# Performance work log

Measured on AMD Instinct MI355X. Metric: run time of the kernel, lower is better.

Reference implementation:

```python
import jax, jax.numpy as jnp
import numpy as np
from jax import lax

P = 2        # conv padding = (Fconv-1)//2 with Fconv=5
T = 10       # relaxation steps (args.T)
PRED_T = 6   # pred_inp_size=[6]: store activations after step 6

def rho(x):
    # hard-sigmoid activation used by the EP model
    return jnp.clip(x, 0.0, 1.0)

def conv2d(x, w, b=None):
    # x: [B,Cin,H,W], w: [Cout,Cin,k,k]
    y = lax.conv_general_dilated(x, w, (1, 1), [(P, P), (P, P)],
                                 dimension_numbers=('NCHW', 'OIHW', 'NCHW'))
    return y if b is None else y + b[None, :, None, None]

def maxpool2x2(x):
    # non-overlapping 2x2 max pool with per-window argmax indices
    B, C, H, W = x.shape
    xr = x.reshape(B, C, H // 2, 2, W // 2, 2).transpose(0, 1, 2, 4, 3, 5)
    xr = xr.reshape(B, C, H // 2, W // 2, 4)
    return jnp.max(xr, axis=-1), jnp.argmax(xr, axis=-1)

def unpool2x2(x, idx):
    # scatter pooled values back to the argmax position in each 2x2 window
    B, C, h, w = x.shape
    y = x[..., None] * jax.nn.one_hot(idx, 4, dtype=x.dtype)  # [B,C,h,w,4]
    return y.reshape(B, C, h, w, 2, 2).transpose(0, 1, 2, 4, 3, 5).reshape(B, C, 2 * h, 2 * w)

def _run(data, s0, s1, s2, conv0_w, conv0_b, conv1_w, conv1_b, fc_w, fc_b):
    B = data.shape[0]
    # conv_transpose2d(x, W, padding=P) == conv2d(x, flip(W).swap(O,I), padding=k-1-P); k=5,P=2 -> pad 2
    tw = jnp.flip(conv0_w, (2, 3)).transpose(1, 0, 2, 3)  # [Cin=64, Cout=128, 5, 5]
    st0 = st1 = st2 = None
    for t in range(T):
        # all dsdt computed from the pre-update states (as in torch stepper)
        d0 = -s0 + rho(s1.reshape(B, -1) @ fc_w.T + fc_b)
        p1, idx1 = maxpool2x2(conv2d(s2, conv0_w, conv0_b))            # [B,128,8,8]
        d1 = -s1 + rho(p1 + (s0 @ fc_w).reshape(s1.shape))              # top-down via fc weight
        p2, _ = maxpool2x2(conv2d(data, conv1_w, conv1_b))             # [B,64,16,16]
        up = conv2d(unpool2x2(s1, idx1), tw)                            # unpool->conv_transpose, [B,64,16,16]
        d2 = -s2 + rho(p2 + up)
        s0, s1, s2 = s0 + d0, s1 + d1, s2 + d2
        if t == PRED_T:  # store_all_activations at pred_inp_size steps
            st0, st1, st2 = s0[..., None], s1[..., None], s2[..., None]
    return s0, s1, s2, st0, st1, st2

def setup_inputs():
    key = jax.random.key(0)
    ks = jax.random.split(key, 6)
    B = 64
    f32 = jnp.float32
    return {
        'data': jax.random.normal(ks[0], (B, 3, 32, 32), f32),
        's0': jnp.zeros((B, 10), f32),
        's1': jnp.zeros((B, 128, 8, 8), f32),
        's2': jnp.zeros((B, 64, 16, 16), f32),
        'conv0_w': jax.random.normal(ks[1], (128, 64, 5, 5), f32) * 0.025,   # ~1/sqrt(64*25)
        'conv0_b': jax.random.normal(ks[2], (128,), f32) * 0.01,
        'conv1_w': jax.random.normal(ks[3], (64, 3, 5, 5), f32) * 0.115,     # ~1/sqrt(75)
        'conv1_b': jax.random.normal(ks[4], (64,), f32) * 0.01,
        'fc_w': jax.random.normal(ks[5], (10, 8192), f32) * 0.011,           # ~1/sqrt(8192)
        'fc_b': jnp.zeros((10,), f32),
    }

def reference(data, s0, s1, s2, conv0_w, conv0_b, conv1_w, conv1_b, fc_w, fc_b):
    return _run(data, s0, s1, s2, conv0_w, conv0_b, conv1_w, conv1_b, fc_w, fc_b)
```

## Files before the change

### kernel.cpp

```cpp
#include <hip/hip_runtime.h>


typedef _Float16 half8 __attribute__((ext_vector_type(8)));
typedef _Float16 half4 __attribute__((ext_vector_type(4)));
typedef _Float16 half2v __attribute__((ext_vector_type(2)));
typedef float f32x4 __attribute__((ext_vector_type(4)));
#define MFMA_F16(A, B, C) __builtin_amdgcn_mfma_f32_16x16x32_f16((A), (B), (C), 0, 0, 0)
#define LO_SCALE 2.44140625e-4f

static __device__ __forceinline__ float rho_(float x) {
  return fminf(fmaxf(x, 0.0f), 1.0f);
}
static __device__ __forceinline__ void split2(float v, _Float16& h, _Float16& l) {
  if (fabsf(v) < 6.1035156e-5f) {
    h = (_Float16)0.f;
    l = (_Float16)(v * 4096.f);
  } else {
    h = (_Float16)v;
    l = (_Float16)((v - (float)h) * 4096.f);
  }
}

__global__ __launch_bounds__(256) void k_wprep(
    const float* __restrict__ w0, const float* __restrict__ fcb,
    const float* __restrict__ fcw,
    _Float16* __restrict__ wA0h, _Float16* __restrict__ wA0l,
    _Float16* __restrict__ wA1h, _Float16* __restrict__ wA1l,
    float* __restrict__ fcwp, float* __restrict__ s0part) {
  int i = blockIdx.x * 256 + threadIdx.x;
  if (i >= 204800) return;
  if (i < 10240) {
    int k = i - (i / 10) * 10;
    s0part[i] = (i < 640) ? -fcb[k] : 0.f;
  }
  if (i < 98304) {
    int jj = i / 12, k = i - jj * 12;
    int cgpyq = jj >> 10, idx = jj & 1023;
    int cgp = cgpyq >> 2, yq = cgpyq & 3;
    int co = idx & 31, win = (idx >> 5) & 15, cgl2 = idx >> 9;
    int co_g = cgp * 64 + cgl2 * 32 + co;
    int phl = win >> 3, pw = win & 7;
    int ph = yq * 2 + phl;
    int j = co_g * 64 + ph * 8 + pw;
    fcwp[i] = (k < 10) ? fcw[k * 8192 + j] : 0.f;
  }
  {
    int cik = i & 31, t1 = i >> 5;
    int co = t1 & 127, t2 = t1 >> 7;
    int ck = t2 & 1, tap = t2 >> 1;
    float v = w0[(co * 64 + ck * 32 + cik) * 25 + tap];
    _Float16 h, l; split2(v, h, l);
    wA0h[i] = h; wA0l[i] = l;
  }
  {
    int cpk = i & 31, t1 = i >> 5;
    int o = t1 & 63, t2 = t1 >> 6;
    int c = t2 & 3, tap = t2 >> 2;
    float v = w0[((c * 32 + cpk) * 64 + o) * 25 + tap];
    _Float16 h, l; split2(v, h, l);
    wA1h[i] = h; wA1l[i] = l;
  }
}

__global__ __launch_bounds__(256) void k_p2(
    const float* __restrict__ data, const float* __restrict__ w,
    const float* __restrict__ bias, float* __restrict__ p2t) {
  __shared__ float ld[3][36][36];
  __shared__ float lw[16][80];
  __shared__ float lb[16];
  int b = blockIdx.x, cg = blockIdx.y, tid = threadIdx.x;
  for (int i = tid; i < 3 * 36 * 36; i += 256) {
    int ci = i / 1296, rem = i % 1296, y = rem / 36, x = rem % 36;
    int gy = y - 2, gx = x - 2;
    float v = 0.f;
    if (gy >= 0 && gy < 32 && gx >= 0 && gx < 32)
      v = data[(b * 3 + ci) * 1024 + gy * 32 + gx];
    ld[ci][y][x] = v;
  }
  for (int i = tid; i < 16 * 75; i += 256) {
    int co = i / 75, k = i % 75;
    lw[co][k] = w[(cg * 16 + co) * 75 + k];
  }
  if (tid < 16) lb[tid] = bias[cg * 16 + tid];
  __syncthreads();
  int ph = tid >> 4, pw = tid & 15;
  int ry = 2 * ph, rx = 2 * pw;
  for (int co = 0; co < 16; co++) {
    float bv = lb[co];
    float a00 = bv, a01 = bv, a10 = bv, a11 = bv;
    for (int ci = 0; ci < 3; ci++) {
#pragma unroll
      for (int ky = 0; ky < 5; ky++) {
#pragma unroll
        for (int kx = 0; kx < 5; kx++) {
          float wv = lw[co][(ci * 5 + ky) * 5 + kx];
          a00 += wv * ld[ci][ry + ky][rx + kx];
          a01 += wv * ld[ci][ry + ky][rx + kx + 1];
          a10 += wv * ld[ci][ry + ky + 1][rx + kx];
          a11 += wv * ld[ci][ry + ky + 1][rx + kx + 1];
        }
      }
    }
    float m = fmaxf(fmaxf(a00, a01), fmaxf(a10, a11));
    p2t[b * 16384 + tid * 64 + cg * 16 + co] = m;
  }
}

__global__ __launch_bounds__(512, 4) void k_conv0F(
    const unsigned* __restrict__ s2pk,
    const _Float16* __restrict__ wA0h, const _Float16* __restrict__ wA0l,
    const float* __restrict__ b0,
    const float* __restrict__ s1old,
    const float* __restrict__ s0prevPart, float* __restrict__ s0curPart,
    const float* __restrict__ fcb,
    const float* __restrict__ fcwp, float* __restrict__ s1new,
    float* __restrict__ s1out,
    unsigned* __restrict__ u) {
  __shared__ __align__(16) _Float16 sm[18576];
  __shared__ float s0l[10];
  __shared__ float s0red[8][10];
  int b = blockIdx.x, cgp = blockIdx.y, yq = blockIdx.z, tid = threadIdx.x;

  if (tid < 10) {
    float s = 0.f;
#pragma unroll
    for (int sl = 0; sl < 8; sl++) s += s0prevPart[(sl * 64 + b) * 10 + tid];
    s0l[tid] = rho_(s + fcb[tid]);
  }

#pragma unroll
  for (int it = 0; it < 4; it++) {
    int idx = it * 512 + tid;
    int ci4 = (idx & 15) * 4;
    int pos = idx >> 4;
    int gy = yq * 4 - 2 + (pos >> 4);
    int lx = pos & 15;
    uint4 pk = {0u, 0u, 0u, 0u};
    if ((unsigned)gy < 16u) pk = *(const uint4*)&s2pk[b * 16384 + (gy * 16 + lx) * 64 + ci4];
    half2v h0 = __builtin_bit_cast(half2v, pk.x);
    half2v h1 = __builtin_bit_cast(half2v, pk.y);
    half2v h2 = __builtin_bit_cast(half2v, pk.z);
    half2v h3 = __builtin_bit_cast(half2v, pk.w);
    half4 hi, lo;
    hi[0] = h0[0]; hi[1] = h1[0]; hi[2] = h2[0]; hi[3] = h3[0];
    lo[0] = h0[1]; lo[1] = h1[1]; lo[2] = h2[1]; lo[3] = h3[1];
    *(half4*)(sm + pos * 72 + ci4) = hi;
    *(half4*)(sm + 9288 + pos * 72 + ci4) = lo;
  }
  if (tid < 72) {
    sm[9216 + tid] = (_Float16)0.f;
    sm[9288 + 9216 + tid] = (_Float16)0.f;
  }
  __syncthreads();

  int lane = tid & 63, w = tid >> 6;
  int kc = w & 1, cgl = (w >> 1) & 1, tg = w >> 2;
  int l16 = lane & 15, quad = lane >> 4;

  f32x4 acch[4][2], accl[4][2];
#pragma unroll
  for (int nt = 0; nt < 4; nt++)
#pragma unroll
    for (int mt = 0; mt < 2; mt++) {
      f32x4 z; z[0] = 0.f; z[1] = 0.f; z[2] = 0.f; z[3] = 0.f;
      acch[nt][mt] = z; accl[nt][mt] = z;
    }

  const int bofs = kc * 32 + quad * 8;
  const int Abase = (kc * 128 + (cgp * 2 + cgl) * 32 + l16) * 32 + quad * 8;
  const int tapLo = tg ? 13 : 0;
  const int tapEnd = tg ? 25 : 13;

  half8 ahc[2], alc[2];
#pragma unroll
  for (int mt = 0; mt < 2; mt++) {
    ahc[mt] = *(const half8*)(wA0h + Abase + tapLo * 8192 + mt * 512);
    alc[mt] = *(const half8*)(wA0l + Abase + tapLo * 8192 + mt * 512);
  }

  for (int tap = tapLo; tap < tapEnd; tap++) {
    half8 ahn[2], aln[2];
    {
      int tn = (tap + 1 < tapEnd) ? tap + 1 : tap;
#pragma unroll
      for (int mt = 0; mt < 2; mt++) {
        ahn[mt] = *(const half8*)(wA0h + Abase + tn * 8192 + mt * 512);
        aln[mt] = *(const half8*)(wA0l + Abase + tn * 8192 + mt * 512);
      }
    }
    int ky = tap / 5, kx = tap - ky * 5;
    int ix = l16 + kx - 2;
    bool oob = ((unsigned)ix > 15u);
#pragma unroll
    for (int nt = 0; nt < 4; nt++) {
      int pos = (nt + ky) * 16 + ix;
      if (oob) pos = 128;
      const _Float16* bp = sm + pos * 72 + bofs;
      half8 bh = *(const half8*)bp;
      half8 bl = *(const half8*)(bp + 9288);
#pragma unroll
      for (int mt = 0; mt < 2; mt++) {
        acch[nt][mt] = MFMA_F16(ahc[mt], bh, acch[nt][mt]);
        accl[nt][mt] = MFMA_F16(alc[mt], bh, accl[nt][mt]);
        accl[nt][mt] = MFMA_F16(ahc[mt], bl, accl[nt][mt]);
      }
    }
#pragma unroll
    for (int mt = 0; mt < 2; mt++) { ahc[mt] = ahn[mt]; alc[mt] = aln[mt]; }
  }

  __syncthreads();
  float* C = (float*)sm;
  if (kc == 1) {
    float* Cw = C + (cgl * 2 + tg) * 2144;
#pragma unroll
    for (int nt = 0; nt < 4; nt++) {
      int pos = nt * 16 + l16;
#pragma unroll
      for (int mt = 0; mt < 2; mt++)
#pragma unroll
        for (int r = 0; r < 4; r++)
          Cw[(mt * 16 + quad * 4 + r) * 67 + pos] = acch[nt][mt][r] + LO_SCALE * accl[nt][mt][r];
    }
  }
  __syncthreads();
  if (kc == 0) {
    float* Cw = C + (cgl * 2 + tg) * 2144;
#pragma unroll
    for (int nt = 0; nt < 4; nt++) {
      int pos = nt * 16 + l16;
#pragma unroll
      for (int mt = 0; mt < 2; mt++)
#pragma unroll
        for (int r = 0; r < 4; r++) {
          int a = (mt * 16 + quad * 4 + r) * 67 + pos;
          Cw[a] += acch[nt][mt][r] + LO_SCALE * accl[nt][mt][r];
        }
    }
  }
  __syncthreads();

  float pacc[10];
#pragma unroll
  for (int k = 0; k < 10; k++) pacc[k] = 0.f;

#pragma unroll
  for (int it2 = 0; it2 < 2; it2++) {
    int idx = it2 * 512 + tid;
    int co = idx & 31, win = (idx >> 5) & 15, cgl2 = idx >> 9;
    int phl = win >> 3, pw = win & 7;
    int p0 = phl * 32 + pw * 2;
    int cbase = cgl2 * 4288;
    int co_g = cgp * 64 + cgl2 * 32 + co;
    float bv = b0[co_g];
    float v[4];
#pragma unroll
    for (int q = 0; q < 4; q++) {
      int ci = co * 67 + p0 + (q >> 1) * 16 + (q & 1);
      float s = C[cbase + ci] + C[cbase + 2144 + ci];
      v[q] = s + bv;
    }
    float m0 = v[0]; int id = 0;
    if (v[1] > m0) { m0 = v[1]; id = 1; }
    if (v[2] > m0) { m0 = v[2]; id = 2; }
    if (v[3] > m0) { m0 = v[3]; id = 3; }
    int ph = yq * 2 + phl;
    int jj = ((cgp * 4 + yq) << 10) + idx;
    int j = co_g * 64 + ph * 8 + pw;
    float sv = s1old[b * 8192 + jj];
    const float4* fp = (const float4*)(fcwp + jj * 12);
    float4 f0 = fp[0], f1 = fp[1], f2 = fp[2];
    float wv[10] = {f0.x, f0.y, f0.z, f0.w, f1.x, f1.y, f1.z, f1.w, f2.x, f2.y};
    float a = m0;
#pragma unroll
    for (int k = 0; k < 10; k++) {
      a += s0l[k] * wv[k];
      pacc[k] += sv * wv[k];
    }
    float r1 = rho_(a);
    s1new[b * 8192 + jj] = r1;
    if (s1out) s1out[b * 8192 + j] = r1;
    _Float16 hh, hl; split2(sv, hh, hl);
    half2v hv; hv[0] = hh; hv[1] = hl;
    unsigned pk = __builtin_bit_cast(unsigned, hv);
    int bu = (b * 256 + ph * 32 + pw * 2) * 128 + co_g;
    u[bu]        = (id == 0) ? pk : 0u;
    u[bu + 128]  = (id == 1) ? pk : 0u;
    u[bu + 2048] = (id == 2) ? pk : 0u;
    u[bu + 2176] = (id == 3) ? pk : 0u;
  }

#pragma unroll
  for (int k = 0; k < 10; k++) {
    float vv = pacc[k];
#pragma unroll
    for (int off = 32; off > 0; off >>= 1) vv += __shfl_xor(vv, off);
    if (lane == 0) s0red[w][k] = vv;
  }
  __syncthreads();
  if (tid < 10) {
    float s = s0red[0][tid] + s0red[1][tid] + s0red[2][tid] + s0red[3][tid]
            + s0red[4][tid] + s0red[5][tid] + s0red[6][tid] + s0red[7][tid];
    s0curPart[((cgp * 4 + yq) * 64 + b) * 10 + tid] = s;
  }
}

__global__ __launch_bounds__(512, 4) void k_convTF(
    const unsigned* __restrict__ u,
    const _Float16* __restrict__ wA1h, const _Float16* __restrict__ wA1l,
    const float* __restrict__ p2t, unsigned* __restrict__ s2pk) {
  __shared__ __align__(16) _Float16 sm[35088];
  int b = blockIdx.x, oh = blockIdx.y, yq = blockIdx.z, tid = threadIdx.x;

#pragma unroll
  for (int it = 0; it < 8; it++) {
    int idx = it * 512 + tid;
    int cp4 = (idx & 31) * 4;
    int pl = idx >> 5;
    int gy = yq * 4 - 2 + (pl >> 4);
    int lx = pl & 15;
    uint4 pk = {0u, 0u, 0u, 0u};
    if ((unsigned)gy < 16u) pk = *(const uint4*)&u[b * 32768 + (gy * 16 + lx) * 128 + cp4];
    half2v h0 = __builtin_bit_cast(half2v, pk.x);
    half2v h1 = __builtin_bit_cast(half2v, pk.y);
    half2v h2 = __builtin_bit_cast(half2v, pk.z);
    half2v h3 = __builtin_bit_cast(half2v, pk.w);
    half4 hi, lo;
    hi[0] = h0[0]; hi[1] = h1[0]; hi[2] = h2[0]; hi[3] = h3[0];
    lo[0] = h0[1]; lo[1] = h1[1]; lo[2] = h2[1]; lo[3] = h3[1];
    *(half4*)(sm + pl * 136 + cp4) = hi;
    *(half4*)(sm + 17544 + pl * 136 + cp4) = lo;
  }
  if (tid < 68) {
    ((unsigned*)sm)[8704 + tid] = 0u;
    ((unsigned*)sm)[8772 + 8704 + tid] = 0u;
  }
  __syncthreads();

  int lane = tid & 63, w = tid >> 6;
  int kc = w & 1, tg = w >> 1;
  int l16 = lane & 15, quad = lane >> 4;

  f32x4 acch[4][2], accl[4][2];
#pragma unroll
  for (int nt = 0; nt < 4; nt++)
#pragma unroll
    for (int mt = 0; mt < 2; mt++) {
      f32x4 z; z[0] = 0.f; z[1] = 0.f; z[2] = 0.f; z[3] = 0.f;
      acch[nt][mt] = z; accl[nt][mt] = z;
    }

  const int Aoff = (oh * 32 + l16) * 32 + quad * 8;
  const int bofs = kc * 64 + quad * 8;
  const int tapLo = (tg == 0) ? 0 : 1 + 6 * tg;
  const int itBeg = tapLo * 2;
  const int itEnd = (tapLo + ((tg == 0) ? 7 : 6)) * 2;

  half8 ahc[2], alc[2];
  {
    int Ab = (tapLo * 4 + kc * 2) * 2048;
#pragma unroll
    for (int mt = 0; mt < 2; mt++) {
      ahc[mt] = *(const half8*)(wA1h + Ab + Aoff + mt * 512);
      alc[mt] = *(const half8*)(wA1l + Ab + Aoff + mt * 512);
    }
  }

  for (int it = itBeg; it < itEnd; it++) {
    half8 ahn[2], aln[2];
    {
      int itn = (it + 1 < itEnd) ? it + 1 : it;
      int Abn = ((itn >> 1) * 4 + kc * 2 + (itn & 1)) * 2048;
#pragma unroll
      for (int mt = 0; mt < 2; mt++) {
        ahn[mt] = *(const half8*)(wA1h + Abn + Aoff + mt * 512);
        aln[mt] = *(const half8*)(wA1l + Abn + Aoff + mt * 512);
      }
    }
    int tap = it >> 1, cs = it & 1;
    int ky = tap / 5, kx = tap - ky * 5;
    int ix = l16 + 2 - kx;
    bool oob = ((unsigned)ix > 15u);
#pragma unroll
    for (int nt = 0; nt < 4; nt++) {
      int pos = (nt + 4 - ky) * 16 + ix;
      if (oob) pos = 128;
      const _Float16* bp = sm + pos * 136 + bofs + cs * 32;
      half8 bh = *(const half8*)bp;
      half8 bl = *(const half8*)(bp + 17544);
#pragma unroll
      for (int mt = 0; mt < 2; mt++) {
        acch[nt][mt] = MFMA_F16(ahc[mt], bh, acch[nt][mt]);
        accl[nt][mt] = MFMA_F16(alc[mt], bh, accl[nt][mt]);
        accl[nt][mt] = MFMA_F16(ahc[mt], bl, accl[nt][mt]);
      }
    }
#pragma unroll
    for (int mt = 0; mt < 2; mt++) { ahc[mt] = ahn[mt]; alc[mt] = aln[mt]; }
  }

  __syncthreads();
  float* C = (float*)sm;
  if (w >= 4) {
    float* Cw = C + (w - 4) * 2144;
#pragma unroll
    for (int nt = 0; nt < 4; nt++) {
      int pos = nt * 16 + l16;
#pragma unroll
      for (int mt = 0; mt < 2; mt++)
#pragma unroll
        for (int r = 0; r < 4; r++)
          Cw[(mt * 16 + quad * 4 + r) * 67 + pos] = acch[nt][mt][r] + LO_SCALE * accl[nt][mt][r];
    }
  }
  __syncthreads();
  if (w < 4) {
    float* Cw = C + w * 2144;
#pragma unroll
    for (int nt = 0; nt < 4; nt++) {
      int pos = nt * 16 + l16;
#pragma unroll
      for (int mt = 0; mt < 2; mt++)
#pragma unroll
        for (int r = 0; r < 4; r++) {
          int a = (mt * 16 + quad * 4 + r) * 67 + pos;
          Cw[a] += acch[nt][mt][r] + LO_SCALE * accl[nt][mt][r];
        }
    }
  }
  __syncthreads();

  int gbase = b * 16384 + yq * 4096 + oh * 32;
#pragma unroll
  for (int it = 0; it < 4; it++) {
    int m = it * 512 + tid;
    int o = m & 31, posl = m >> 5;
    int ci = o * 67 + posl;
    float s = C[ci] + C[ci + 2144] + C[ci + 4288] + C[ci + 6432];
    int gi = gbase + posl * 64 + o;
    float v = rho_(p2t[gi] + s);
    _Float16 h, l; split2(v, h, l);
    half2v hv; hv[0] = h; hv[1] = l;
    s2pk[gi] = __builtin_bit_cast(unsigned, hv);
  }
}

__global__ __launch_bounds__(256) void k_cTcomb(
    const unsigned* __restrict__ s2pk, float* __restrict__ out_s2,
    const float* __restrict__ s0part, const float* __restrict__ fcb,
    float* __restrict__ out_s0) {
  int blk = blockIdx.x, tid = threadIdx.x;
  if (blk < 256) {
    __shared__ float tl[64 * 65];
    int b = blk >> 2, pt = blk & 3;
    for (int it = 0; it < 16; it++) {
      int idx = it * 256 + tid;
      int ci = idx & 63, posl = idx >> 6;
      unsigned pk = s2pk[b * 16384 + (pt * 64 + posl) * 64 + ci];
      half2v hv = __builtin_bit_cast(half2v, pk);
      tl[posl * 65 + ci] = (float)hv[0] + LO_SCALE * (float)hv[1];
    }
    __syncthreads();
    for (int it = 0; it < 16; it++) {
      int idx = it * 256 + tid;
      int posl = idx & 63, ci = idx >> 6;
      out_s2[b * 16384 + ci * 256 + pt * 64 + posl] = tl[posl * 65 + ci];
    }
  } else {
    int i = (blk - 256) * 256 + tid;
    if (i < 640) {
      int bb = i / 10, k = i - bb * 10;
      float s = 0.f;
#pragma unroll
      for (int sl = 0; sl < 8; sl++) s += s0part[(sl * 64 + bb) * 10 + k];
      out_s0[i] = rho_(s + fcb[k]);
    }
  }
}

extern "C" void kernel_launch(void* const* d_in, const int* in_sizes, int n_in,
                              void* d_out, int out_size, void* d_ws, size_t ws_size,
                              hipStream_t stream) {
  const float* data   = (const float*)d_in[0];
  const float* s0init = (const float*)d_in[1];
  const float* s1init = (const float*)d_in[2];
  const float* s2init = (const float*)d_in[3];
  const float* conv0w = (const float*)d_in[4];
  const float* conv0b = (const float*)d_in[5];
  const float* conv1w = (const float*)d_in[6];
  const float* conv1b = (const float*)d_in[7];
  const float* fcw    = (const float*)d_in[8];
  const float* fcb    = (const float*)d_in[9];
  (void)s0init; (void)s2init;

  float* p = (float*)d_ws;
  float* s0part = p;                         p += 10240;
  float* s1buf[2] = {p, p + 524288};         p += 1048576;
  float* p2t = p;                            p += 1048576;
  float* fcwp = p;                           p += 98304;
  unsigned* u = (unsigned*)p;                p += 2097152;
  unsigned* s2pk = (unsigned*)p;             p += 1048576;
  _Float16* hq = (_Float16*)p;
  _Float16* wA0h = hq;                       hq += 204800;
  _Float16* wA0l = hq;                       hq += 204800;
  _Float16* wA1h = hq;                       hq += 204800;
  _Float16* wA1l = hq;                       hq += 204800;

  hipMemsetAsync(s2pk, 0, 1048576 * sizeof(unsigned), stream);
  k_wprep<<<800, 256, 0, stream>>>(conv0w, fcb, fcw, wA0h, wA0l, wA1h, wA1l, fcwp, s0part);
  k_p2<<<dim3(64, 4), 256, 0, stream>>>(data, conv1w, conv1b, p2t);

  const float* s1o = s1init;
  float* outp = (float*)d_out;

  for (int t = 0; t < 10; t++) {
    int nb = t & 1;
    float* s1w = s1buf[nb];
    float* s1out = (t == 6) ? (outp + 1574144) : ((t == 9) ? (outp + 640) : nullptr);

    k_conv0F<<<dim3(64, 2, 4), 512, 0, stream>>>(s2pk,
                                                 wA0h, wA0l, conv0b,
                                                 s1o,
                                                 s0part + (t & 1) * 5120,
                                                 s0part + ((t + 1) & 1) * 5120,
                                                 fcb, fcwp, s1w, s1out, u);
    k_convTF<<<dim3(64, 2, 4), 512, 0, stream>>>(u, wA1h, wA1l, p2t, s2pk);

    s1o = s1w;

    if (t == 6) {
      k_cTcomb<<<259, 256, 0, stream>>>(s2pk, outp + 2098432,
                                        s0part + 5120, fcb, outp + 1573504);
    }
  }

  k_cTcomb<<<259, 256, 0, stream>>>(s2pk, outp + 524928,
                                    s0part, fcb, outp + 0);
}
```

Measured before the change: 520.7 us.

## Fold prep kernels, memset and output combine kernels into the main conv kernels

Merges the memset, weight-prep and p2 conv kernels into one prep launch. The separate combine kernels that wrote the s2 and s0 outputs are removed: k_convTF now writes the fp32 s2 output directly, and the s0 snapshots are computed inside k_conv0F and k_convTF. This cuts several launches and an extra pass over s2, in exchange for scattered, uncoalesced s2out stores and extra branches in the hot kernels.

```diff
diff --git a/kernel.cpp b/kernel.cpp
--- a/kernel.cpp
+++ b/kernel.cpp
@@ -21,54 +21,57 @@
   }
 }
 
-__global__ __launch_bounds__(256) void k_wprep(
+__global__ __launch_bounds__(256) void k_prep(
     const float* __restrict__ w0, const float* __restrict__ fcb,
     const float* __restrict__ fcw,
+    const float* __restrict__ data, const float* __restrict__ conv1w,
+    const float* __restrict__ conv1b,
     _Float16* __restrict__ wA0h, _Float16* __restrict__ wA0l,
     _Float16* __restrict__ wA1h, _Float16* __restrict__ wA1l,
-    float* __restrict__ fcwp, float* __restrict__ s0part) {
-  int i = blockIdx.x * 256 + threadIdx.x;
-  if (i >= 204800) return;
-  if (i < 10240) {
-    int k = i - (i / 10) * 10;
-    s0part[i] = (i < 640) ? -fcb[k] : 0.f;
-  }
-  if (i < 98304) {
-    int jj = i / 12, k = i - jj * 12;
-    int cgpyq = jj >> 10, idx = jj & 1023;
-    int cgp = cgpyq >> 2, yq = cgpyq & 3;
-    int co = idx & 31, win = (idx >> 5) & 15, cgl2 = idx >> 9;
-    int co_g = cgp * 64 + cgl2 * 32 + co;
-    int phl = win >> 3, pw = win & 7;
-    int ph = yq * 2 + phl;
-    int j = co_g * 64 + ph * 8 + pw;
-    fcwp[i] = (k < 10) ? fcw[k * 8192 + j] : 0.f;
-  }
-  {
-    int cik = i & 31, t1 = i >> 5;
-    int co = t1 & 127, t2 = t1 >> 7;
-    int ck = t2 & 1, tap = t2 >> 1;
-    float v = w0[(co * 64 + ck * 32 + cik) * 25 + tap];
-    _Float16 h, l; split2(v, h, l);
-    wA0h[i] = h; wA0l[i] = l;
-  }
-  {
-    int cpk = i & 31, t1 = i >> 5;
-    int o = t1 & 63, t2 = t1 >> 6;
-    int c = t2 & 3, tap = t2 >> 2;
-    float v = w0[((c * 32 + cpk) * 64 + o) * 25 + tap];
-    _Float16 h, l; split2(v, h, l);
-    wA1h[i] = h; wA1l[i] = l;
-  }
-}
-
-__global__ __launch_bounds__(256) void k_p2(
-    const float* __restrict__ data, const float* __restrict__ w,
-    const float* __restrict__ bias, float* __restrict__ p2t) {
+    float* __restrict__ fcwp, float* __restrict__ s0part,
+    float* __restrict__ p2t, unsigned* __restrict__ s2pk) {
   __shared__ float ld[3][36][36];
   __shared__ float lw[16][80];
   __shared__ float lb[16];
-  int b = blockIdx.x, cg = blockIdx.y, tid = threadIdx.x;
+  int blk = blockIdx.x, tid = threadIdx.x;
+  if (blk < 800) {
+    int i = blk * 256 + tid;
+    for (int j = i; j < 1048576; j += 204800) s2pk[j] = 0u;
+    if (i < 10240) {
+      int k = i - (i / 10) * 10;
+      s0part[i] = (i < 640) ? -fcb[k] : 0.f;
+    }
+    if (i < 98304) {
+      int jj = i / 12, k = i - jj * 12;
+      int cgpyq = jj >> 10, idx = jj & 1023;
+      int cgp = cgpyq >> 2, yq = cgpyq & 3;
+      int co = idx & 31, win = (idx >> 5) & 15, cgl2 = idx >> 9;
+      int co_g = cgp * 64 + cgl2 * 32 + co;
+      int phl = win >> 3, pw = win & 7;
+      int ph = yq * 2 + phl;
+      int j = co_g * 64 + ph * 8 + pw;
+      fcwp[i] = (k < 10) ? fcw[k * 8192 + j] : 0.f;
+    }
+    {
+      int cik = i & 31, t1 = i >> 5;
+      int co = t1 & 127, t2 = t1 >> 7;
+      int ck = t2 & 1, tap = t2 >> 1;
+      float v = w0[(co * 64 + ck * 32 + cik) * 25 + tap];
+      _Float16 h, l; split2(v, h, l);
+      wA0h[i] = h; wA0l[i] = l;
+    }
+    {
+      int cpk = i & 31, t1 = i >> 5;
+      int o = t1 & 63, t2 = t1 >> 6;
+      int c = t2 & 3, tap = t2 >> 2;
+      float v = w0[((c * 32 + cpk) * 64 + o) * 25 + tap];
+      _Float16 h, l; split2(v, h, l);
+      wA1h[i] = h; wA1l[i] = l;
+    }
+    return;
+  }
+  int pb = blk - 800;
+  int b = pb >> 2, cg = pb & 3;
   for (int i = tid; i < 3 * 36 * 36; i += 256) {
     int ci = i / 1296, rem = i % 1296, y = rem / 36, x = rem % 36;
     int gy = y - 2, gx = x - 2;
@@ -79,9 +82,9 @@
   }
   for (int i = tid; i < 16 * 75; i += 256) {
     int co = i / 75, k = i % 75;
-    lw[co][k] = w[(cg * 16 + co) * 75 + k];
-  }
-  if (tid < 16) lb[tid] = bias[cg * 16 + tid];
+    lw[co][k] = conv1w[(cg * 16 + co) * 75 + k];
+  }
+  if (tid < 16) lb[tid] = conv1b[cg * 16 + tid];
   __syncthreads();
   int ph = tid >> 4, pw = tid & 15;
   int ry = 2 * ph, rx = 2 * pw;
@@ -114,7 +117,7 @@
     const float* __restrict__ s0prevPart, float* __restrict__ s0curPart,
     const float* __restrict__ fcb,
     const float* __restrict__ fcwp, float* __restrict__ s1new,
-    float* __restrict__ s1out,
+    float* __restrict__ s1out, float* __restrict__ s0snap,
     unsigned* __restrict__ u) {
   __shared__ __align__(16) _Float16 sm[18576];
   __shared__ float s0l[10];
@@ -125,7 +128,9 @@
     float s = 0.f;
 #pragma unroll
     for (int sl = 0; sl < 8; sl++) s += s0prevPart[(sl * 64 + b) * 10 + tid];
-    s0l[tid] = rho_(s + fcb[tid]);
+    float v = rho_(s + fcb[tid]);
+    s0l[tid] = v;
+    if (s0snap && cgp == 0 && yq == 0) s0snap[b * 10 + tid] = v;
   }
 
 #pragma unroll
@@ -308,9 +313,19 @@
 __global__ __launch_bounds__(512, 4) void k_convTF(
     const unsigned* __restrict__ u,
     const _Float16* __restrict__ wA1h, const _Float16* __restrict__ wA1l,
-    const float* __restrict__ p2t, unsigned* __restrict__ s2pk) {
+    const float* __restrict__ p2t, unsigned* __restrict__ s2pk,
+    float* __restrict__ s2out,
+    const float* __restrict__ s0partCur, const float* __restrict__ fcb,
+    float* __restrict__ s0fin) {
   __shared__ __align__(16) _Float16 sm[35088];
   int b = blockIdx.x, oh = blockIdx.y, yq = blockIdx.z, tid = threadIdx.x;
+
+  if (s0fin && oh == 0 && yq == 0 && tid < 10) {
+    float s = 0.f;
+#pragma unroll
+    for (int sl = 0; sl < 8; sl++) s += s0partCur[(sl * 64 + b) * 10 + tid];
+    s0fin[b * 10 + tid] = rho_(s + fcb[tid]);
+  }
 
 #pragma unroll
   for (int it = 0; it < 8; it++) {
@@ -442,39 +457,7 @@
     _Float16 h, l; split2(v, h, l);
     half2v hv; hv[0] = h; hv[1] = l;
     s2pk[gi] = __builtin_bit_cast(unsigned, hv);
-  }
-}
-
-__global__ __launch_bounds__(256) void k_cTcomb(
-    const unsigned* __restrict__ s2pk, float* __restrict__ out_s2,
-    const float* __restrict__ s0part, const float* __restrict__ fcb,
-    float* __restrict__ out_s0) {
-  int blk = blockIdx.x, tid = threadIdx.x;
-  if (blk < 256) {
-    __shared__ float tl[64 * 65];
-    int b = blk >> 2, pt = blk & 3;
-    for (int it = 0; it < 16; it++) {
-      int idx = it * 256 + tid;
-      int ci = idx & 63, posl = idx >> 6;
-      unsigned pk = s2pk[b * 16384 + (pt * 64 + posl) * 64 + ci];
-      half2v hv = __builtin_bit_cast(half2v, pk);
-      tl[posl * 65 + ci] = (float)hv[0] + LO_SCALE * (float)hv[1];
-    }
-    __syncthreads();
-    for (int it = 0; it < 16; it++) {
-      int idx = it * 256 + tid;
-      int posl = idx & 63, ci = idx >> 6;
-      out_s2[b * 16384 + ci * 256 + pt * 64 + posl] = tl[posl * 65 + ci];
-    }
-  } else {
-    int i = (blk - 256) * 256 + tid;
-    if (i < 640) {
-      int bb = i / 10, k = i - bb * 10;
-      float s = 0.f;
-#pragma unroll
-      for (int sl = 0; sl < 8; sl++) s += s0part[(sl * 64 + bb) * 10 + k];
-      out_s0[i] = rho_(s + fcb[k]);
-    }
+    if (s2out) s2out[b * 16384 + (oh * 32 + o) * 256 + yq * 64 + posl] = v;
   }
 }
 
@@ -506,9 +489,8 @@
   _Float16* wA1h = hq;                       hq += 204800;
   _Float16* wA1l = hq;                       hq += 204800;
 
-  hipMemsetAsync(s2pk, 0, 1048576 * sizeof(unsigned), stream);
-  k_wprep<<<800, 256, 0, stream>>>(conv0w, fcb, fcw, wA0h, wA0l, wA1h, wA1l, fcwp, s0part);
-  k_p2<<<dim3(64, 4), 256, 0, stream>>>(data, conv1w, conv1b, p2t);
+  k_prep<<<1056, 256, 0, stream>>>(conv0w, fcb, fcw, data, conv1w, conv1b,
+                                   wA0h, wA0l, wA1h, wA1l, fcwp, s0part, p2t, s2pk);
 
   const float* s1o = s1init;
   float* outp = (float*)d_out;
@@ -517,23 +499,21 @@
     int nb = t & 1;
     float* s1w = s1buf[nb];
     float* s1out = (t == 6) ? (outp + 1574144) : ((t == 9) ? (outp + 640) : nullptr);
+    float* s0snap = (t == 7) ? (outp + 1573504) : nullptr;
 
     k_conv0F<<<dim3(64, 2, 4), 512, 0, stream>>>(s2pk,
                                                  wA0h, wA0l, conv0b,
                                                  s1o,
                                                  s0part + (t & 1) * 5120,
                                                  s0part + ((t + 1) & 1) * 5120,
-                                                 fcb, fcwp, s1w, s1out, u);
-    k_convTF<<<dim3(64, 2, 4), 512, 0, stream>>>(u, wA1h, wA1l, p2t, s2pk);
+                                                 fcb, fcwp, s1w, s1out, s0snap, u);
+    float* s2out = (t == 6) ? (outp + 2098432) : ((t == 9) ? (outp + 524928) : nullptr);
+    float* s0fin = (t == 9) ? outp : nullptr;
+    k_convTF<<<dim3(64, 2, 4), 512, 0, stream>>>(u, wA1h, wA1l, p2t, s2pk,
+                                                 s2out,
+                                                 s0part + ((t + 1) & 1) * 5120, fcb,
+                                                 s0fin);
 
     s1o = s1w;
-
-    if (t == 6) {
-      k_cTcomb<<<259, 256, 0, stream>>>(s2pk, outp + 2098432,
-                                        s0part + 5120, fcb, outp + 1573504);
-    }
-  }
-
-  k_cTcomb<<<259, 256, 0, stream>>>(s2pk, outp + 524928,
-                                    s0part, fcb, outp + 0);
+  }
 }
```

Measured after the change: 534.9 us. +2.7%, slower.
